# Kernel optimization log

Measured on AMD Instinct MI355X. Metric: run time of the kernel, lower is better.

## Reference

```python
import jax, jax.numpy as jnp
import numpy as np

N_NODES = 100000
N_EDGES = 1600000
F_IN = 64
C = 128          # hidden_encoding == element_embedding
STEPS = 4
NEG_SLOPE = 0.01  # torch.nn.LeakyReLU default


def setup_inputs() -> dict:
    key = jax.random.key(0)
    ks = jax.random.split(key, 8)
    s = 0.05
    return {
        "x": jax.random.normal(ks[0], (N_NODES, F_IN), dtype=jnp.float32),
        "edge_index": jax.random.randint(ks[1], (2, N_EDGES), 0, N_NODES, dtype=jnp.int64),
        "W_in": jax.random.normal(ks[2], (C, F_IN), dtype=jnp.float32) * s,
        "W_mpnn": jax.random.normal(ks[3], (STEPS, C, C), dtype=jnp.float32) * s,
        "W_ih": jax.random.normal(ks[4], (3 * C, C), dtype=jnp.float32) * s,
        "W_hh": jax.random.normal(ks[5], (3 * C, C), dtype=jnp.float32) * s,
        "b_ih": jnp.zeros((3 * C,), dtype=jnp.float32),
        "b_hh": jnp.zeros((3 * C,), dtype=jnp.float32),
        "W_pred": jax.random.normal(ks[6], (1, C), dtype=jnp.float32) * s,
        "b_pred": jnp.zeros((1,), dtype=jnp.float32),
    }


def reference(x, edge_index, W_in, W_mpnn, W_ih, W_hh, b_ih, b_hh, W_pred, b_pred):
    src, dst = edge_index[0], edge_index[1]
    n = x.shape[0]
    # input embedding (bias=False)
    h = x @ W_in.T                                  # [N, C]
    for i in range(STEPS):
        m = h @ W_mpnn[i]                           # [N, C] (PyG: matmul(x, weight[i]))
        agg = jax.ops.segment_sum(m[src], dst, num_segments=n)  # scatter-add aggr
        # torch GRUCell, gate order r, z, n
        gi = agg @ W_ih.T + b_ih                    # [N, 3C]
        gh = h @ W_hh.T + b_hh                      # [N, 3C]
        r = jax.nn.sigmoid(gi[:, :C] + gh[:, :C])
        z = jax.nn.sigmoid(gi[:, C:2 * C] + gh[:, C:2 * C])
        nn_ = jnp.tanh(gi[:, 2 * C:] + r * gh[:, 2 * C:])
        h = (1.0 - z) * nn_ + z * h
    h = jnp.where(h >= 0, h, NEG_SLOPE * h)         # LeakyReLU
    g = jnp.mean(h, axis=0)                         # graph readout [C]
    return g @ W_pred.T + b_pred                    # [1]
```

## Files before the change

### kernel.cpp

```cpp
#include <hip/hip_runtime.h>
#include <cstdint>

typedef __attribute__((ext_vector_type(8))) short bf16x8;
typedef __attribute__((ext_vector_type(4))) float f32x4;
typedef __attribute__((address_space(1))) unsigned int ga_u32;
typedef __attribute__((address_space(3))) unsigned int ls_u32;

__device__ __forceinline__ float bf2f(unsigned short u) {
    union { unsigned int i; float f; } v; v.i = ((unsigned int)u) << 16; return v.f;
}
__device__ __forceinline__ float bfhi(unsigned int w) {
    union { unsigned int i; float f; } v; v.i = w & 0xffff0000u; return v.f;
}
__device__ __forceinline__ float bflo(unsigned int w) {
    union { unsigned int i; float f; } v; v.i = w << 16; return v.f;
}
__device__ __forceinline__ unsigned short f2bf(float f) {
    union { float ff; unsigned int i; } v; v.ff = f;
    unsigned int r = (v.i + 0x7fffu + ((v.i >> 16) & 1u)) >> 16;
    return (unsigned short)r;
}
__device__ __forceinline__ int origcol(int nc) {
    int w = nc / 96, rem = nc % 96, g = rem / 32, cc = rem % 32;
    return g * 128 + w * 32 + cc;
}

__global__ void detect_kernel(const unsigned int* __restrict__ x32,
                              const int* __restrict__ ei32,
                              int* __restrict__ flags)
{
    __shared__ int insaneS;
    __shared__ int orS;
    int tid = threadIdx.x;
    if (tid == 0) { insaneS = 0; orS = 0; }
    __syncthreads();
    int insane = 0;
    for (int j = tid; j < 512; j += 256) {
        unsigned int w = x32[j];
        int e = (int)((w >> 7) & 0xFF);
        if (e > 135 || e < 100) insane++;
    }
    int ov = 0;
    for (int j = tid; j < 256; j += 256) ov |= ei32[2 * j + 1];
    atomicAdd(&insaneS, insane);
    atomicOr(&orS, ov);
    __syncthreads();
    if (tid == 0) {
        flags[0] = (insaneS < 64) ? 1 : 0;
        flags[1] = (orS == 0) ? 1 : 0;
    }
}

__global__ void convall_kernel(const void* W_in, const void* W_mpnn, const void* W_ih,
                               const void* W_hh, const void* b_ih, const void* b_hh,
                               const void* W_pred, const void* b_pred,
                               float* __restrict__ Winf, float* __restrict__ Wmf,
                               float* __restrict__ Wihf, float* __restrict__ Whhf,
                               float* __restrict__ bihf, float* __restrict__ bhhf,
                               float* __restrict__ Wpf, float* __restrict__ bpf,
                               int steps, const int* __restrict__ flags)
{
    int i = blockIdx.x * 256 + threadIdx.x;
    int bf = flags[0];
    auto get = [&](const void* p, int idx) -> float {
        return bf ? bf2f(((const unsigned short*)p)[idx]) : ((const float*)p)[idx];
    };
    int n0 = 8192, n1 = n0 + steps * 16384, n2 = n1 + 49152, n3 = n2 + 49152;
    int n4 = n3 + 384, n5 = n4 + 384, n6 = n5 + 128, n7 = n6 + 1;
    if      (i < n0) Winf[i]      = get(W_in,   i);
    else if (i < n1) Wmf[i - n0]  = get(W_mpnn, i - n0);
    else if (i < n2) Wihf[i - n1] = get(W_ih,   i - n1);
    else if (i < n3) Whhf[i - n2] = get(W_hh,   i - n2);
    else if (i < n4) bihf[i - n3] = get(b_ih,   i - n3);
    else if (i < n5) bhhf[i - n4] = get(b_hh,   i - n4);
    else if (i < n6) Wpf[i - n5]  = get(W_pred, i - n5);
    else if (i < n7) bpf[i - n6]  = get(b_pred, i - n6);
}

__global__ void wcomb_kernel(const float* __restrict__ Wm,
                             const float* __restrict__ Wih,
                             float* __restrict__ Wcomb, int steps)
{
    int i = blockIdx.x * 256 + threadIdx.x;
    int total = steps * 49152;
    if (i >= total) return;
    int step = i / 49152;
    int rem = i - step * 49152;
    int k = rem / 384;
    int j = rem - k * 384;
    const float* wm = Wm + ((long)step * 128 + k) * 128;
    const float* wi = Wih + (long)j * 128;
    float s = 0.f;
#pragma unroll 8
    for (int t = 0; t < 128; ++t) s += wm[t] * wi[t];
    Wcomb[i] = s;
}

__global__ void pack_gates(const float* __restrict__ Wcomb,
                           const float* __restrict__ Whhf,
                           const float* __restrict__ bihf, const float* __restrict__ bhhf,
                           unsigned short* __restrict__ Bci,
                           unsigned short* __restrict__ Bhh,
                           float* __restrict__ bip, float* __restrict__ bhp,
                           int steps)
{
    int i = blockIdx.x * 256 + threadIdx.x;
    int nmat = steps * 49152;
    if (i < nmat) {
        int s = i / 49152, r = i - s * 49152;
        int t = r >> 11, rem = r & 2047;
        int ks = rem >> 9, l = (rem >> 3) & 63, j = rem & 7;
        int k = ks * 32 + (l >> 4) * 8 + j;
        int oc = origcol(t * 16 + (l & 15));
        Bci[i] = f2bf(Wcomb[(long)s * 49152 + k * 384 + oc]);
    } else if (i < nmat + 49152) {
        int r = i - nmat;
        int t = r >> 11, rem = r & 2047;
        int ks = rem >> 9, l = (rem >> 3) & 63, j = rem & 7;
        int k = ks * 32 + (l >> 4) * 8 + j;
        int oc = origcol(t * 16 + (l & 15));
        Bhh[r] = f2bf(Whhf[(long)oc * 128 + k]);
    } else if (i < nmat + 49152 + 768) {
        int b = i - nmat - 49152;
        if (b < 384) bip[b] = bihf[origcol(b)];
        else         bhp[b - 384] = bhhf[origcol(b - 384)];
    }
}

__global__ void pack_in(const float* __restrict__ Winf, unsigned short* __restrict__ Bin)
{
    int r = blockIdx.x * 256 + threadIdx.x;
    if (r >= 8192) return;
    int t = r >> 10, rem = r & 1023;
    int ks = rem >> 9, l = (rem >> 3) & 63, j = rem & 7;
    int k = ks * 32 + (l >> 4) * 8 + j;
    int col = t * 16 + (l & 15);
    Bin[r] = f2bf(Winf[col * 64 + k]);
}

__global__ __launch_bounds__(256) void gemm_in(const void* __restrict__ xraw,
                        const int* __restrict__ flags,
                        const unsigned short* __restrict__ Bin,
                        unsigned short* __restrict__ hout, int N)
{
    const int w = threadIdx.x >> 6, lane = threadIdx.x & 63;
    const int m = lane & 15, quad = lane >> 4;
    const int rowBase = blockIdx.x * 32;
    const bool abf = flags[0] != 0;
    f32x4 acc[2][2];
#pragma unroll
    for (int rt = 0; rt < 2; ++rt)
#pragma unroll
        for (int ct = 0; ct < 2; ++ct) acc[rt][ct] = (f32x4){0.f, 0.f, 0.f, 0.f};

#pragma unroll
    for (int ks = 0; ks < 2; ++ks) {
        bf16x8 a[2];
#pragma unroll
        for (int rt = 0; rt < 2; ++rt) {
            long row = rowBase + rt * 16 + m;
            if (abf) {
                a[rt] = *(const bf16x8*)(const void*)((const unsigned short*)xraw + row * 64 + ks * 32 + quad * 8);
            } else {
                const float* xp = (const float*)xraw + row * 64 + ks * 32 + quad * 8;
                float4 f0 = *(const float4*)xp;
                float4 f1 = *(const float4*)(xp + 4);
                bf16x8 t;
                t[0] = (short)f2bf(f0.x); t[1] = (short)f2bf(f0.y);
                t[2] = (short)f2bf(f0.z); t[3] = (short)f2bf(f0.w);
                t[4] = (short)f2bf(f1.x); t[5] = (short)f2bf(f1.y);
                t[6] = (short)f2bf(f1.z); t[7] = (short)f2bf(f1.w);
                a[rt] = t;
            }
        }
#pragma unroll
        for (int ct = 0; ct < 2; ++ct) {
            int t = w * 2 + ct;
            bf16x8 b = *(const bf16x8*)(const void*)(Bin + ((t * 2 + ks) * 64 + lane) * 8);
#pragma unroll
            for (int rt = 0; rt < 2; ++rt)
                acc[rt][ct] = __builtin_amdgcn_mfma_f32_16x16x32_bf16(a[rt], b, acc[rt][ct], 0, 0, 0);
        }
    }
#pragma unroll
    for (int rt = 0; rt < 2; ++rt)
#pragma unroll
        for (int ct = 0; ct < 2; ++ct)
#pragma unroll
            for (int reg = 0; reg < 4; ++reg) {
                int row = rowBase + rt * 16 + quad * 4 + reg;
                int col = w * 32 + ct * 16 + m;
                if (row < N) hout[(long)row * 128 + col] = f2bf(acc[rt][ct][reg]);
            }
}

__global__ __launch_bounds__(512, 2) void step_kernel(
    const unsigned short* __restrict__ hin,
    const unsigned short* __restrict__ aggb,
    const unsigned short* __restrict__ Bci,
    const unsigned short* __restrict__ Bhh,
    const float* __restrict__ bip, const float* __restrict__ bhp,
    unsigned short* __restrict__ hout, int N, int ntiles)
{
    __shared__ unsigned short lds[16384];
    const int tid = threadIdx.x;
    const int w = tid >> 6, lane = tid & 63;
    const int m = lane & 15, quad = lane >> 4;
    const int cg = w >> 1, half = w & 1;
    const int col = cg * 32 + half * 16 + m;
    const int grid = gridDim.x;

    bf16x8 bI[4][3], bH[4][3];
#pragma unroll
    for (int ks = 0; ks < 4; ++ks)
#pragma unroll
        for (int g = 0; g < 3; ++g) {
            int t = cg * 6 + g * 2 + half;
            bI[ks][g] = *(const bf16x8*)(const void*)(Bci + (((long)t * 4 + ks) * 64 + lane) * 8);
            bH[ks][g] = *(const bf16x8*)(const void*)(Bhh + (((long)t * 4 + ks) * 64 + lane) * 8);
        }
    float bi0[3], bh0[3];
#pragma unroll
    for (int g = 0; g < 3; ++g) {
        int nc = (cg * 6 + g * 2 + half) * 16 + m;
        bi0[g] = bip[nc]; bh0[g] = bhp[nc];
    }

    const int lrow = w * 4 + (lane >> 4);
    const int schunk = (lane & 15) ^ (lrow & 7);

    long tile = blockIdx.x;
    int cur = 0;
    if (tile < ntiles) {
        const unsigned short* gap = aggb + (tile * 32 + lrow) * 128 + schunk * 8;
        const unsigned short* ghp = hin  + (tile * 32 + lrow) * 128 + schunk * 8;
        __builtin_amdgcn_global_load_lds((const ga_u32*)gap, (ls_u32*)(lds + w * 512), 16, 0, 0);
        __builtin_amdgcn_global_load_lds((const ga_u32*)ghp, (ls_u32*)(lds + 4096 + w * 512), 16, 0, 0);
    }

    for (; tile < ntiles; tile += grid) {
        long nxt = tile + grid;
        bool hasNext = nxt < ntiles;
        if (hasNext) {
            int nb = cur ^ 1;
            const unsigned short* gap = aggb + (nxt * 32 + lrow) * 128 + schunk * 8;
            const unsigned short* ghp = hin  + (nxt * 32 + lrow) * 128 + schunk * 8;
            __builtin_amdgcn_global_load_lds((const ga_u32*)gap, (ls_u32*)(lds + nb * 8192 + w * 512), 16, 0, 0);
            __builtin_amdgcn_global_load_lds((const ga_u32*)ghp, (ls_u32*)(lds + nb * 8192 + 4096 + w * 512), 16, 0, 0);
            asm volatile("s_waitcnt vmcnt(2)" ::: "memory");
        } else {
            asm volatile("s_waitcnt vmcnt(0)" ::: "memory");
        }
        __builtin_amdgcn_s_barrier();

        const unsigned short* abuf = lds + cur * 8192;
        const unsigned short* hbuf = lds + cur * 8192 + 4096;

        f32x4 gi[2][3], gh[2][3];
#pragma unroll
        for (int g = 0; g < 3; ++g)
#pragma unroll
            for (int rt = 0; rt < 2; ++rt) {
                gi[rt][g] = (f32x4){bi0[g], bi0[g], bi0[g], bi0[g]};
                gh[rt][g] = (f32x4){bh0[g], bh0[g], bh0[g], bh0[g]};
            }

#pragma unroll
        for (int ks = 0; ks < 4; ++ks) {
            bf16x8 aA[2], hA[2];
#pragma unroll
            for (int rt = 0; rt < 2; ++rt) {
                int r = rt * 16 + m;
                int ch = (ks * 4 + quad) ^ (r & 7);
                aA[rt] = *(const bf16x8*)(const void*)(abuf + r * 128 + ch * 8);
                hA[rt] = *(const bf16x8*)(const void*)(hbuf + r * 128 + ch * 8);
            }
#pragma unroll
            for (int g = 0; g < 3; ++g)
#pragma unroll
                for (int rt = 0; rt < 2; ++rt) {
                    gi[rt][g] = __builtin_amdgcn_mfma_f32_16x16x32_bf16(aA[rt], bI[ks][g], gi[rt][g], 0, 0, 0);
                    gh[rt][g] = __builtin_amdgcn_mfma_f32_16x16x32_bf16(hA[rt], bH[ks][g], gh[rt][g], 0, 0, 0);
                }
        }

        long rowBase = tile * 32;
#pragma unroll
        for (int rt = 0; rt < 2; ++rt)
#pragma unroll
            for (int reg = 0; reg < 4; ++reg) {
                long row = rowBase + rt * 16 + quad * 4 + reg;
                if (row < N) {
                    int r2 = rt * 16 + quad * 4 + reg;
                    int hidx = r2 * 128 + ((((col >> 3) ^ (r2 & 7)) << 3) + (col & 7));
                    float R  = __builtin_amdgcn_rcpf(1.f + __expf(-(gi[rt][0][reg] + gh[rt][0][reg])));
                    float Z  = __builtin_amdgcn_rcpf(1.f + __expf(-(gi[rt][1][reg] + gh[rt][1][reg])));
                    float u  = gi[rt][2][reg] + R * gh[rt][2][reg];
                    float e2 = __expf(-2.f * fabsf(u));
                    float Nn = copysignf((1.f - e2) * __builtin_amdgcn_rcpf(1.f + e2), u);
                    float hold = bf2f(hbuf[hidx]);
                    hout[row * 128 + col] = f2bf((1.f - Z) * Nn + Z * hold);
                }
            }

        __builtin_amdgcn_s_barrier();
        cur ^= 1;
    }
}

__global__ __launch_bounds__(256) void part1_kernel(
    const int* __restrict__ ei, int E, const int* __restrict__ flags,
    int* __restrict__ gcnt, uint2* __restrict__ pair2,
    int nb, int cshift, int ccap, int chunk)
{
    __shared__ int cnt[256];
    __shared__ int base_s[256];
    const int tid = threadIdx.x;
    if (tid < nb) cnt[tid] = 0;
    __syncthreads();
    const bool i64 = flags[1] != 0;
    const long long* e64 = (const long long*)ei;
    int lo = blockIdx.x * chunk;
    int hi = lo + chunk; if (hi > E) hi = E;
    for (int i = lo + tid; i < hi; i += 256) {
        int d = i64 ? (int)e64[(long)E + i] : ei[(long)E + i];
        atomicAdd(&cnt[d >> cshift], 1);
    }
    __syncthreads();
    if (tid < nb) {
        int c = cnt[tid];
        base_s[tid] = (c > 0) ? atomicAdd(&gcnt[tid], c) : 0;
        cnt[tid] = 0;
    }
    __syncthreads();
    for (int i = lo + tid; i < hi; i += 256) {
        int s, d;
        if (i64) { s = (int)e64[i]; d = (int)e64[(long)E + i]; }
        else     { s = ei[i];       d = ei[(long)E + i]; }
        int c = d >> cshift;
        int p = base_s[c] + atomicAdd(&cnt[c], 1);
        if (p < ccap) { uint2 pr; pr.x = (unsigned)s; pr.y = (unsigned)d; pair2[(long)c * ccap + p] = pr; }
    }
}

__global__ void scanco_kernel(const int* __restrict__ gcnt, int* __restrict__ cbase,
                              int nb, int ccap)
{
    __shared__ int wsum[4];
    int tid = threadIdx.x, lane = tid & 63, wv = tid >> 6;
    int x = (tid < nb) ? gcnt[tid] : 0;
    if (x > ccap) x = ccap;
    int inc = x;
#pragma unroll
    for (int d = 1; d < 64; d <<= 1) { int u = __shfl_up(inc, d); if (lane >= d) inc += u; }
    if (lane == 63) wsum[wv] = inc;
    __syncthreads();
    if (tid == 0) { int s = 0; for (int q = 0; q < 4; ++q) { int t = wsum[q]; wsum[q] = s; s += t; } }
    __syncthreads();
    int excl = wsum[wv] + inc - x;
    if (tid < nb) cbase[tid] = excl;
    if (tid == nb - 1) cbase[nb] = excl + x;
}

__global__ __launch_bounds__(256) void part2_kernel(
    const uint2* __restrict__ pair2, const int* __restrict__ gcnt,
    const int* __restrict__ cbase,
    int* __restrict__ offs, int* __restrict__ csr,
    int N, int nb, int cshift, int ccap)
{
    __shared__ int lb[2048];
    __shared__ int wsum[4];
    const int b = blockIdx.x, tid = threadIdx.x;
    const int span = 1 << cshift;
    const int n0 = b << cshift;
    int count = gcnt[b]; if (count > ccap) count = ccap;
    for (int k = tid; k < span; k += 256) lb[k] = 0;
    __syncthreads();
    const uint2* pp = pair2 + (long)b * ccap;
    for (int i = tid; i < count; i += 256)
        atomicAdd(&lb[(int)pp[i].y - n0], 1);
    __syncthreads();
    int npe = span >> 8; if (npe < 1) npe = 1;
    int myb = tid * npe;
    int vals[8];
    int sum = 0;
    for (int k = 0; k < npe; ++k) { vals[k] = lb[myb + k]; sum += vals[k]; }
    int lane = tid & 63, wv = tid >> 6;
    int inc = sum;
#pragma unroll
    for (int d = 1; d < 64; d <<= 1) { int u = __shfl_up(inc, d); if (lane >= d) inc += u; }
    if (lane == 63) wsum[wv] = inc;
    __syncthreads();
    if (tid == 0) { int s = 0; for (int q = 0; q < 4; ++q) { int t = wsum[q]; wsum[q] = s; s += t; } }
    __syncthreads();
    int run = wsum[wv] + inc - sum;
    __syncthreads();
    for (int k = 0; k < npe; ++k) { lb[myb + k] = run; run += vals[k]; }
    __syncthreads();
    int gb = cbase[b];
    int nn = N - n0; if (nn > span) nn = span;
    for (int g = tid; g < nn; g += 256) offs[n0 + g] = gb + lb[g];
    if (b == nb - 1 && tid == 0) offs[N] = cbase[nb];
    __syncthreads();
    for (int i = tid; i < count; i += 256) {
        uint2 pr = pp[i];
        int p = gb + atomicAdd(&lb[(int)pr.y - n0], 1);
        csr[p] = (int)pr.x;
    }
}

__global__ __launch_bounds__(256) void aggregate(const unsigned short* __restrict__ hb,
                          const int* __restrict__ off,
                          const int* __restrict__ csr,
                          unsigned short* __restrict__ aggb, int n)
{
    int wv = threadIdx.x >> 6, lane = threadIdx.x & 63;
    int slot = lane >> 4;
    int c16 = lane & 15;
    int nw = gridDim.x * 4;
    int wid = blockIdx.x * 4 + wv;
    int chunk = (n + nw - 1) / nw;
    int lo = wid * chunk;
    int hi = lo + chunk; if (hi > n) hi = n;

    for (int node = lo; node < hi; ++node) {
        int s0 = off[node], s1 = off[node + 1];
        float a0 = 0.f, a1 = 0.f, a2 = 0.f, a3 = 0.f, a4 = 0.f, a5 = 0.f, a6 = 0.f, a7 = 0.f;
        if (s1 > s0) {
            int last = s1 - 1;
            for (int j = s0 + slot; j < s1; j += 16) {
                uint4 vv[4];
                float wt[4];
#pragma unroll
                for (int t = 0; t < 4; ++t) {
                    int jj = j + 4 * t;
                    int idx = csr[jj <= last ? jj : last];
                    vv[t] = *(const uint4*)(const void*)(hb + (long)idx * 128 + c16 * 8);
                    wt[t] = (jj <= last) ? 1.f : 0.f;
                }
#pragma unroll
                for (int t = 0; t < 4; ++t) {
                    a0 = fmaf(bflo(vv[t].x), wt[t], a0);
                    a1 = fmaf(bfhi(vv[t].x), wt[t], a1);
                    a2 = fmaf(bflo(vv[t].y), wt[t], a2);
                    a3 = fmaf(bfhi(vv[t].y), wt[t], a3);
                    a4 = fmaf(bflo(vv[t].z), wt[t], a4);
                    a5 = fmaf(bfhi(vv[t].z), wt[t], a5);
                    a6 = fmaf(bflo(vv[t].w), wt[t], a6);
                    a7 = fmaf(bfhi(vv[t].w), wt[t], a7);
                }
            }
        }
        a0 += __shfl_xor(a0, 16); a1 += __shfl_xor(a1, 16);
        a2 += __shfl_xor(a2, 16); a3 += __shfl_xor(a3, 16);
        a4 += __shfl_xor(a4, 16); a5 += __shfl_xor(a5, 16);
        a6 += __shfl_xor(a6, 16); a7 += __shfl_xor(a7, 16);
        a0 += __shfl_xor(a0, 32); a1 += __shfl_xor(a1, 32);
        a2 += __shfl_xor(a2, 32); a3 += __shfl_xor(a3, 32);
        a4 += __shfl_xor(a4, 32); a5 += __shfl_xor(a5, 32);
        a6 += __shfl_xor(a6, 32); a7 += __shfl_xor(a7, 32);
        if (slot == 0) {
            uint4 o;
            o.x = ((unsigned int)f2bf(a1) << 16) | f2bf(a0);
            o.y = ((unsigned int)f2bf(a3) << 16) | f2bf(a2);
            o.z = ((unsigned int)f2bf(a5) << 16) | f2bf(a4);
            o.w = ((unsigned int)f2bf(a7) << 16) | f2bf(a6);
            *(uint4*)(void*)(aggb + (long)node * 128 + c16 * 8) = o;
        }
    }
}

__global__ void colsum(const unsigned short* __restrict__ hb, float* __restrict__ acc, int n) {
    int c = threadIdx.x & 127;
    int sub = threadIdx.x >> 7;
    float local = 0.f;
    for (long r = blockIdx.x * 2 + sub; r < n; r += (long)gridDim.x * 2) {
        float v = bf2f(hb[r * 128 + c]);
        local += (v >= 0.f) ? v : 0.01f * v;
    }
    atomicAdd(&acc[c], local);
}

__global__ void finalize(const float* __restrict__ acc,
                         const float* __restrict__ W_pred_f,
                         const float* __restrict__ b_pred_f,
                         unsigned int* __restrict__ out, float invN)
{
    __shared__ float ws2[2];
    int t = threadIdx.x;
    float v = acc[t] * invN * W_pred_f[t];
#pragma unroll
    for (int d = 32; d >= 1; d >>= 1) v += __shfl_down(v, d);
    if ((t & 63) == 0) ws2[t >> 6] = v;
    __syncthreads();
    if (t == 0) {
        float r = ws2[0] + ws2[1] + b_pred_f[0];
        unsigned int bf = (unsigned int)f2bf(r);
        out[0] = (bf << 16) | bf;
    }
}

extern "C" void kernel_launch(void* const* d_in, const int* in_sizes, int n_in,
                              void* d_out, int out_size, void* d_ws, size_t ws_size,
                              hipStream_t stream)
{
    const void* x      = d_in[0];
    const int*  ei     = (const int*)d_in[1];
    const void* W_in   = d_in[2];
    const void* W_mpnn = d_in[3];
    const void* W_ih   = d_in[4];
    const void* W_hh   = d_in[5];
    const void* b_ih   = d_in[6];
    const void* b_hh   = d_in[7];
    const void* W_pred = d_in[8];
    const void* b_pred = d_in[9];

    const int N = in_sizes[0] / 64;
    const int E = in_sizes[1] / 2;
    const int STEPS = in_sizes[3] / (128 * 128);

    int cshift = 9;
    while ((((N + (1 << cshift) - 1) >> cshift)) > 256 && cshift < 11) cshift++;
    const int NCO = (N + (1 << cshift) - 1) >> cshift;
    const int ccap = (((E / NCO) * 3 / 2 + 1024) + 255) & ~255;
    const int chunk = (E + 255) / 256;

    size_t woff = 0;
    auto carve = [&](size_t bytes) -> void* {
        void* p = (char*)d_ws + woff;
        woff = (woff + bytes + 255) & ~(size_t)255;
        return p;
    };
    int*   flags = (int*)carve(2 * 4);
    float* Winf  = (float*)carve(8192 * 4);
    float* Wmf   = (float*)carve((size_t)STEPS * 16384 * 4);
    float* Wihf  = (float*)carve(49152 * 4);
    float* Whhf  = (float*)carve(49152 * 4);
    float* bihf  = (float*)carve(384 * 4);
    float* bhhf  = (float*)carve(384 * 4);
    float* Wpf   = (float*)carve(128 * 4);
    float* bpf   = (float*)carve(4);
    float* Wcomb = (float*)carve((size_t)STEPS * 49152 * 4);
    unsigned short* Bci = (unsigned short*)carve((size_t)STEPS * 49152 * 2);
    unsigned short* Bhh = (unsigned short*)carve(49152 * 2);
    unsigned short* Bin = (unsigned short*)carve(8192 * 2);
    float* bip   = (float*)carve(384 * 4);
    float* bhp   = (float*)carve(384 * 4);
    unsigned short* hA   = (unsigned short*)carve(((size_t)N * 128 + 16384) * 2);
    unsigned short* hB   = (unsigned short*)carve(((size_t)N * 128 + 16384) * 2);
    unsigned short* aggb = (unsigned short*)carve(((size_t)N * 128 + 16384) * 2);
    int*   gcnt  = (int*)carve(256 * 4);
    int*   cbase = (int*)carve(257 * 4);
    int*   offs  = (int*)carve((size_t)(N + 1) * 4);
    int*   csr   = (int*)carve((size_t)E * 4 + 256);
    uint2* pair2 = (uint2*)carve((size_t)NCO * ccap * 8);
    float* accb  = (float*)carve(128 * 4);

    hipMemsetAsync(gcnt, 0, 256 * 4, stream);
    hipMemsetAsync(accb, 0, 128 * 4, stream);

    detect_kernel<<<1, 256, 0, stream>>>((const unsigned int*)x, ei, flags);

    {
        int total = 8192 + STEPS * 16384 + 2 * 49152 + 768 + 129;
        convall_kernel<<<(total + 255) / 256, 256, 0, stream>>>(
            W_in, W_mpnn, W_ih, W_hh, b_ih, b_hh, W_pred, b_pred,
            Winf, Wmf, Wihf, Whhf, bihf, bhhf, Wpf, bpf, STEPS, flags);
    }

    wcomb_kernel<<<(STEPS * 49152 + 255) / 256, 256, 0, stream>>>(Wmf, Wihf, Wcomb, STEPS);
    {
        int total = (STEPS + 1) * 49152 + 768;
        pack_gates<<<(total + 255) / 256, 256, 0, stream>>>(Wcomb, Whhf, bihf, bhhf,
                                                            Bci, Bhh, bip, bhp, STEPS);
    }
    pack_in<<<32, 256, 0, stream>>>(Winf, Bin);

    gemm_in<<<(N + 31) / 32, 256, 0, stream>>>(x, flags, Bin, hA, N);

    part1_kernel<<<256, 256, 0, stream>>>(ei, E, flags, gcnt, pair2, NCO, cshift, ccap, chunk);
    scanco_kernel<<<1, 256, 0, stream>>>(gcnt, cbase, NCO, ccap);
    part2_kernel<<<NCO, 256, 0, stream>>>(pair2, gcnt, cbase, offs, csr, N, NCO, cshift, ccap);

    int aggBlocks = (N + 3) / 4; if (aggBlocks > 2048) aggBlocks = 2048;
    const int ntiles = (N + 31) / 32;
    int stepBlocks = ntiles < 256 ? ntiles : 256;
    unsigned short* hcur = hA;
    unsigned short* hnxt = hB;
    for (int step = 0; step < STEPS; ++step) {
        aggregate<<<aggBlocks, 256, 0, stream>>>(hcur, offs, csr, aggb, N);
        step_kernel<<<stepBlocks, 512, 0, stream>>>(
            hcur, aggb, Bci + (size_t)step * 49152, Bhh, bip, bhp, hnxt, N, ntiles);
        unsigned short* t = hcur; hcur = hnxt; hnxt = t;
    }

    colsum<<<512, 256, 0, stream>>>(hcur, accb, N);
    finalize<<<1, 128, 0, stream>>>(accb, Wpf, bpf, (unsigned int*)d_out, 1.f / (float)N);
}
```

Baseline: 595.5 us.

## Fuse weight-prep, scan and finalize kernels to cut launch count

Merges detection, weight conversion, Wcomb product and packing into one prep kernel that reads raw weights directly. The block-count scan moves into part2 (each block recomputes it), and the finalize step becomes a last-block-done tail in colsum. Two memsets collapse into one. The aim is to remove about seven small kernel launches and the intermediate fp32 buffers, at the cost of redundant detection work in every prep block and redundant scans in every part2 block.

Result: no change. 602.3 us (+1.1%).

```diff
diff --git a/kernel.cpp b/kernel.cpp
--- a/kernel.cpp
+++ b/kernel.cpp
@@ -25,117 +25,104 @@
     return g * 128 + w * 32 + cc;
 }
 
-__global__ void detect_kernel(const unsigned int* __restrict__ x32,
-                              const int* __restrict__ ei32,
-                              int* __restrict__ flags)
-{
-    __shared__ int insaneS;
-    __shared__ int orS;
-    int tid = threadIdx.x;
+__global__ __launch_bounds__(256) void prep_kernel(
+    const unsigned int* __restrict__ x32, const int* __restrict__ ei32,
+    const void* W_in, const void* W_mpnn, const void* W_ih, const void* W_hh,
+    const void* b_ih, const void* b_hh, const void* W_pred, const void* b_pred,
+    unsigned short* __restrict__ Bci, unsigned short* __restrict__ Bhh,
+    float* __restrict__ bip, float* __restrict__ bhp,
+    unsigned short* __restrict__ Bin,
+    float* __restrict__ Wpf, float* __restrict__ bpf,
+    int* __restrict__ flags, int steps)
+{
+    __shared__ int insaneS, orS;
+    const int tid = threadIdx.x;
     if (tid == 0) { insaneS = 0; orS = 0; }
     __syncthreads();
-    int insane = 0;
-    for (int j = tid; j < 512; j += 256) {
-        unsigned int w = x32[j];
-        int e = (int)((w >> 7) & 0xFF);
-        if (e > 135 || e < 100) insane++;
-    }
-    int ov = 0;
-    for (int j = tid; j < 256; j += 256) ov |= ei32[2 * j + 1];
-    atomicAdd(&insaneS, insane);
-    atomicOr(&orS, ov);
-    __syncthreads();
-    if (tid == 0) {
-        flags[0] = (insaneS < 64) ? 1 : 0;
+    {
+        int insane = 0;
+        for (int j = tid; j < 512; j += 256) {
+            unsigned int w = x32[j];
+            int e = (int)((w >> 7) & 0xFF);
+            if (e > 135 || e < 100) insane++;
+        }
+        int ov = 0;
+        for (int j = tid; j < 256; j += 256) ov |= ei32[2 * j + 1];
+        atomicAdd(&insaneS, insane);
+        atomicOr(&orS, ov);
+    }
+    __syncthreads();
+    const bool bf = insaneS < 64;
+    if (blockIdx.x == 0 && tid == 0) {
+        flags[0] = bf ? 1 : 0;
         flags[1] = (orS == 0) ? 1 : 0;
     }
-}
-
-__global__ void convall_kernel(const void* W_in, const void* W_mpnn, const void* W_ih,
-                               const void* W_hh, const void* b_ih, const void* b_hh,
-                               const void* W_pred, const void* b_pred,
-                               float* __restrict__ Winf, float* __restrict__ Wmf,
-                               float* __restrict__ Wihf, float* __restrict__ Whhf,
-                               float* __restrict__ bihf, float* __restrict__ bhhf,
-                               float* __restrict__ Wpf, float* __restrict__ bpf,
-                               int steps, const int* __restrict__ flags)
-{
-    int i = blockIdx.x * 256 + threadIdx.x;
-    int bf = flags[0];
-    auto get = [&](const void* p, int idx) -> float {
+
+    auto cvt = [&](const void* p, long idx) -> float {
         return bf ? bf2f(((const unsigned short*)p)[idx]) : ((const float*)p)[idx];
     };
-    int n0 = 8192, n1 = n0 + steps * 16384, n2 = n1 + 49152, n3 = n2 + 49152;
-    int n4 = n3 + 384, n5 = n4 + 384, n6 = n5 + 128, n7 = n6 + 1;
-    if      (i < n0) Winf[i]      = get(W_in,   i);
-    else if (i < n1) Wmf[i - n0]  = get(W_mpnn, i - n0);
-    else if (i < n2) Wihf[i - n1] = get(W_ih,   i - n1);
-    else if (i < n3) Whhf[i - n2] = get(W_hh,   i - n2);
-    else if (i < n4) bihf[i - n3] = get(b_ih,   i - n3);
-    else if (i < n5) bhhf[i - n4] = get(b_hh,   i - n4);
-    else if (i < n6) Wpf[i - n5]  = get(W_pred, i - n5);
-    else if (i < n7) bpf[i - n6]  = get(b_pred, i - n6);
-}
-
-__global__ void wcomb_kernel(const float* __restrict__ Wm,
-                             const float* __restrict__ Wih,
-                             float* __restrict__ Wcomb, int steps)
-{
-    int i = blockIdx.x * 256 + threadIdx.x;
-    int total = steps * 49152;
-    if (i >= total) return;
-    int step = i / 49152;
-    int rem = i - step * 49152;
-    int k = rem / 384;
-    int j = rem - k * 384;
-    const float* wm = Wm + ((long)step * 128 + k) * 128;
-    const float* wi = Wih + (long)j * 128;
-    float s = 0.f;
-#pragma unroll 8
-    for (int t = 0; t < 128; ++t) s += wm[t] * wi[t];
-    Wcomb[i] = s;
-}
-
-__global__ void pack_gates(const float* __restrict__ Wcomb,
-                           const float* __restrict__ Whhf,
-                           const float* __restrict__ bihf, const float* __restrict__ bhhf,
-                           unsigned short* __restrict__ Bci,
-                           unsigned short* __restrict__ Bhh,
-                           float* __restrict__ bip, float* __restrict__ bhp,
-                           int steps)
-{
-    int i = blockIdx.x * 256 + threadIdx.x;
-    int nmat = steps * 49152;
-    if (i < nmat) {
-        int s = i / 49152, r = i - s * 49152;
+
+    const long n1 = (long)steps * 49152;
+    const long n2 = n1 + 49152;
+    const long n3 = n2 + 768;
+    const long n4 = n3 + 8192;
+    const long n5 = n4 + 128;
+    long i = (long)blockIdx.x * 256 + tid;
+
+    if (i < n1) {
+        int st = (int)(i / 49152), r = (int)(i - (long)st * 49152);
         int t = r >> 11, rem = r & 2047;
         int ks = rem >> 9, l = (rem >> 3) & 63, j = rem & 7;
         int k = ks * 32 + (l >> 4) * 8 + j;
         int oc = origcol(t * 16 + (l & 15));
-        Bci[i] = f2bf(Wcomb[(long)s * 49152 + k * 384 + oc]);
-    } else if (i < nmat + 49152) {
-        int r = i - nmat;
+        float s = 0.f;
+        if (bf) {
+            const unsigned short* wm = (const unsigned short*)W_mpnn + ((long)st * 128 + k) * 128;
+            const unsigned short* wi = (const unsigned short*)W_ih + (long)oc * 128;
+#pragma unroll 4
+            for (int tt = 0; tt < 128; tt += 8) {
+                uint4 a = *(const uint4*)(const void*)(wm + tt);
+                uint4 b = *(const uint4*)(const void*)(wi + tt);
+                s += bflo(a.x) * bflo(b.x) + bfhi(a.x) * bfhi(b.x);
+                s += bflo(a.y) * bflo(b.y) + bfhi(a.y) * bfhi(b.y);
+                s += bflo(a.z) * bflo(b.z) + bfhi(a.z) * bfhi(b.z);
+                s += bflo(a.w) * bflo(b.w) + bfhi(a.w) * bfhi(b.w);
+            }
+        } else {
+            const float* wm = (const float*)W_mpnn + ((long)st * 128 + k) * 128;
+            const float* wi = (const float*)W_ih + (long)oc * 128;
+#pragma unroll 4
+            for (int tt = 0; tt < 128; tt += 4) {
+                float4 a = *(const float4*)(wm + tt);
+                float4 b = *(const float4*)(wi + tt);
+                s += a.x * b.x + a.y * b.y + a.z * b.z + a.w * b.w;
+            }
+        }
+        Bci[i] = f2bf(s);
+    } else if (i < n2) {
+        int r = (int)(i - n1);
         int t = r >> 11, rem = r & 2047;
         int ks = rem >> 9, l = (rem >> 3) & 63, j = rem & 7;
         int k = ks * 32 + (l >> 4) * 8 + j;
         int oc = origcol(t * 16 + (l & 15));
-        Bhh[r] = f2bf(Whhf[(long)oc * 128 + k]);
-    } else if (i < nmat + 49152 + 768) {
-        int b = i - nmat - 49152;
-        if (b < 384) bip[b] = bihf[origcol(b)];
-        else         bhp[b - 384] = bhhf[origcol(b - 384)];
-    }
-}
-
-__global__ void pack_in(const float* __restrict__ Winf, unsigned short* __restrict__ Bin)
-{
-    int r = blockIdx.x * 256 + threadIdx.x;
-    if (r >= 8192) return;
-    int t = r >> 10, rem = r & 1023;
-    int ks = rem >> 9, l = (rem >> 3) & 63, j = rem & 7;
-    int k = ks * 32 + (l >> 4) * 8 + j;
-    int col = t * 16 + (l & 15);
-    Bin[r] = f2bf(Winf[col * 64 + k]);
+        Bhh[r] = f2bf(cvt(W_hh, (long)oc * 128 + k));
+    } else if (i < n3) {
+        int b = (int)(i - n2);
+        if (b < 384) bip[b] = cvt(b_ih, origcol(b));
+        else         bhp[b - 384] = cvt(b_hh, origcol(b - 384));
+    } else if (i < n4) {
+        int r = (int)(i - n3);
+        int t = r >> 10, rem = r & 1023;
+        int ks = rem >> 9, l = (rem >> 3) & 63, j = rem & 7;
+        int k = ks * 32 + (l >> 4) * 8 + j;
+        int col = t * 16 + (l & 15);
+        Bin[r] = f2bf(cvt(W_in, col * 64 + k));
+    } else if (i < n5) {
+        int idx = (int)(i - n4);
+        Wpf[idx] = cvt(W_pred, idx);
+    } else if (i == n5) {
+        bpf[0] = cvt(b_pred, 0);
+    }
 }
 
 __global__ __launch_bounds__(256) void gemm_in(const void* __restrict__ xraw,
@@ -343,36 +330,35 @@
     }
 }
 
-__global__ void scanco_kernel(const int* __restrict__ gcnt, int* __restrict__ cbase,
-                              int nb, int ccap)
-{
-    __shared__ int wsum[4];
-    int tid = threadIdx.x, lane = tid & 63, wv = tid >> 6;
-    int x = (tid < nb) ? gcnt[tid] : 0;
-    if (x > ccap) x = ccap;
-    int inc = x;
-#pragma unroll
-    for (int d = 1; d < 64; d <<= 1) { int u = __shfl_up(inc, d); if (lane >= d) inc += u; }
-    if (lane == 63) wsum[wv] = inc;
-    __syncthreads();
-    if (tid == 0) { int s = 0; for (int q = 0; q < 4; ++q) { int t = wsum[q]; wsum[q] = s; s += t; } }
-    __syncthreads();
-    int excl = wsum[wv] + inc - x;
-    if (tid < nb) cbase[tid] = excl;
-    if (tid == nb - 1) cbase[nb] = excl + x;
-}
-
 __global__ __launch_bounds__(256) void part2_kernel(
     const uint2* __restrict__ pair2, const int* __restrict__ gcnt,
-    const int* __restrict__ cbase,
     int* __restrict__ offs, int* __restrict__ csr,
     int N, int nb, int cshift, int ccap)
 {
     __shared__ int lb[2048];
     __shared__ int wsum[4];
+    __shared__ int cb[257];
     const int b = blockIdx.x, tid = threadIdx.x;
     const int span = 1 << cshift;
     const int n0 = b << cshift;
+    int lane = tid & 63, wv = tid >> 6;
+
+    {
+        int x = (tid < nb) ? gcnt[tid] : 0;
+        if (x > ccap) x = ccap;
+        int inc = x;
+#pragma unroll
+        for (int d = 1; d < 64; d <<= 1) { int u = __shfl_up(inc, d); if (lane >= d) inc += u; }
+        if (lane == 63) wsum[wv] = inc;
+        __syncthreads();
+        if (tid == 0) { int s = 0; for (int q = 0; q < 4; ++q) { int t = wsum[q]; wsum[q] = s; s += t; } }
+        __syncthreads();
+        int excl = wsum[wv] + inc - x;
+        if (tid < nb) cb[tid] = excl;
+        if (tid == nb - 1) cb[nb] = excl + x;
+    }
+    __syncthreads();
+
     int count = gcnt[b]; if (count > ccap) count = ccap;
     for (int k = tid; k < span; k += 256) lb[k] = 0;
     __syncthreads();
@@ -385,7 +371,6 @@
     int vals[8];
     int sum = 0;
     for (int k = 0; k < npe; ++k) { vals[k] = lb[myb + k]; sum += vals[k]; }
-    int lane = tid & 63, wv = tid >> 6;
     int inc = sum;
 #pragma unroll
     for (int d = 1; d < 64; d <<= 1) { int u = __shfl_up(inc, d); if (lane >= d) inc += u; }
@@ -397,10 +382,10 @@
     __syncthreads();
     for (int k = 0; k < npe; ++k) { lb[myb + k] = run; run += vals[k]; }
     __syncthreads();
-    int gb = cbase[b];
+    int gb = cb[b];
     int nn = N - n0; if (nn > span) nn = span;
     for (int g = tid; g < nn; g += 256) offs[n0 + g] = gb + lb[g];
-    if (b == nb - 1 && tid == 0) offs[N] = cbase[nb];
+    if (b == nb - 1 && tid == 0) offs[N] = cb[nb];
     __syncthreads();
     for (int i = tid; i < count; i += 256) {
         uint2 pr = pp[i];
@@ -470,7 +455,15 @@
     }
 }
 
-__global__ void colsum(const unsigned short* __restrict__ hb, float* __restrict__ acc, int n) {
+__global__ void colsum_fin(const unsigned short* __restrict__ hb,
+                           const float* __restrict__ Wpf,
+                           const float* __restrict__ bpf,
+                           unsigned int* __restrict__ out,
+                           float* __restrict__ acc, int* __restrict__ done,
+                           int n, float invN)
+{
+    __shared__ int isLast;
+    __shared__ float ws2[2];
     int c = threadIdx.x & 127;
     int sub = threadIdx.x >> 7;
     float local = 0.f;
@@ -479,24 +472,27 @@
         local += (v >= 0.f) ? v : 0.01f * v;
     }
     atomicAdd(&acc[c], local);
-}
-
-__global__ void finalize(const float* __restrict__ acc,
-                         const float* __restrict__ W_pred_f,
-                         const float* __restrict__ b_pred_f,
-                         unsigned int* __restrict__ out, float invN)
-{
-    __shared__ float ws2[2];
-    int t = threadIdx.x;
-    float v = acc[t] * invN * W_pred_f[t];
-#pragma unroll
-    for (int d = 32; d >= 1; d >>= 1) v += __shfl_down(v, d);
-    if ((t & 63) == 0) ws2[t >> 6] = v;
-    __syncthreads();
-    if (t == 0) {
-        float r = ws2[0] + ws2[1] + b_pred_f[0];
-        unsigned int bf = (unsigned int)f2bf(r);
-        out[0] = (bf << 16) | bf;
+    __threadfence();
+    if (threadIdx.x == 0) {
+        int d = atomicAdd(done, 1);
+        isLast = (d == (int)gridDim.x - 1) ? 1 : 0;
+    }
+    __syncthreads();
+    if (isLast) {
+        float v = 0.f;
+        if (threadIdx.x < 128) {
+            float a = atomicAdd(&acc[threadIdx.x], 0.f);
+            v = a * invN * Wpf[threadIdx.x];
+        }
+#pragma unroll
+        for (int d = 32; d >= 1; d >>= 1) v += __shfl_down(v, d);
+        if (threadIdx.x < 128 && (threadIdx.x & 63) == 0) ws2[threadIdx.x >> 6] = v;
+        __syncthreads();
+        if (threadIdx.x == 0) {
+            float r = ws2[0] + ws2[1] + bpf[0];
+            unsigned int bfv = (unsigned int)f2bf(r);
+            out[0] = (bfv << 16) | bfv;
+        }
     }
 }
 
@@ -532,15 +528,8 @@
         return p;
     };
     int*   flags = (int*)carve(2 * 4);
-    float* Winf  = (float*)carve(8192 * 4);
-    float* Wmf   = (float*)carve((size_t)STEPS * 16384 * 4);
-    float* Wihf  = (float*)carve(49152 * 4);
-    float* Whhf  = (float*)carve(49152 * 4);
-    float* bihf  = (float*)carve(384 * 4);
-    float* bhhf  = (float*)carve(384 * 4);
     float* Wpf   = (float*)carve(128 * 4);
     float* bpf   = (float*)carve(4);
-    float* Wcomb = (float*)carve((size_t)STEPS * 49152 * 4);
     unsigned short* Bci = (unsigned short*)carve((size_t)STEPS * 49152 * 2);
     unsigned short* Bhh = (unsigned short*)carve(49152 * 2);
     unsigned short* Bin = (unsigned short*)carve(8192 * 2);
@@ -549,38 +538,28 @@
     unsigned short* hA   = (unsigned short*)carve(((size_t)N * 128 + 16384) * 2);
     unsigned short* hB   = (unsigned short*)carve(((size_t)N * 128 + 16384) * 2);
     unsigned short* aggb = (unsigned short*)carve(((size_t)N * 128 + 16384) * 2);
-    int*   gcnt  = (int*)carve(256 * 4);
-    int*   cbase = (int*)carve(257 * 4);
     int*   offs  = (int*)carve((size_t)(N + 1) * 4);
     int*   csr   = (int*)carve((size_t)E * 4 + 256);
     uint2* pair2 = (uint2*)carve((size_t)NCO * ccap * 8);
+    int*   gcnt  = (int*)carve(256 * 4);
     float* accb  = (float*)carve(128 * 4);
-
-    hipMemsetAsync(gcnt, 0, 256 * 4, stream);
-    hipMemsetAsync(accb, 0, 128 * 4, stream);
-
-    detect_kernel<<<1, 256, 0, stream>>>((const unsigned int*)x, ei, flags);
+    int*   done  = (int*)carve(4);
+    size_t zbytes = (size_t)((char*)done - (char*)gcnt) + 256;
+
+    hipMemsetAsync(gcnt, 0, zbytes, stream);
 
     {
-        int total = 8192 + STEPS * 16384 + 2 * 49152 + 768 + 129;
-        convall_kernel<<<(total + 255) / 256, 256, 0, stream>>>(
-            W_in, W_mpnn, W_ih, W_hh, b_ih, b_hh, W_pred, b_pred,
-            Winf, Wmf, Wihf, Whhf, bihf, bhhf, Wpf, bpf, STEPS, flags);
-    }
-
-    wcomb_kernel<<<(STEPS * 49152 + 255) / 256, 256, 0, stream>>>(Wmf, Wihf, Wcomb, STEPS);
-    {
-        int total = (STEPS + 1) * 49152 + 768;
-        pack_gates<<<(total + 255) / 256, 256, 0, stream>>>(Wcomb, Whhf, bihf, bhhf,
-                                                            Bci, Bhh, bip, bhp, STEPS);
-    }
-    pack_in<<<32, 256, 0, stream>>>(Winf, Bin);
+        long total = (long)STEPS * 49152 + 49152 + 768 + 8192 + 128 + 1;
+        int blocks = (int)((total + 255) / 256);
+        prep_kernel<<<blocks, 256, 0, stream>>>(
+            (const unsigned int*)x, ei, W_in, W_mpnn, W_ih, W_hh, b_ih, b_hh,
+            W_pred, b_pred, Bci, Bhh, bip, bhp, Bin, Wpf, bpf, flags, STEPS);
+    }
 
     gemm_in<<<(N + 31) / 32, 256, 0, stream>>>(x, flags, Bin, hA, N);
 
     part1_kernel<<<256, 256, 0, stream>>>(ei, E, flags, gcnt, pair2, NCO, cshift, ccap, chunk);
-    scanco_kernel<<<1, 256, 0, stream>>>(gcnt, cbase, NCO, ccap);
-    part2_kernel<<<NCO, 256, 0, stream>>>(pair2, gcnt, cbase, offs, csr, N, NCO, cshift, ccap);
+    part2_kernel<<<NCO, 256, 0, stream>>>(pair2, gcnt, offs, csr, N, NCO, cshift, ccap);
 
     int aggBlocks = (N + 3) / 4; if (aggBlocks > 2048) aggBlocks = 2048;
     const int ntiles = (N + 31) / 32;
@@ -594,6 +573,6 @@
         unsigned short* t = hcur; hcur = hnxt; hnxt = t;
     }
 
-    colsum<<<512, 256, 0, stream>>>(hcur, accb, N);
-    finalize<<<1, 128, 0, stream>>>(accb, Wpf, bpf, (unsigned int*)d_out, 1.f / (float)N);
-}
+    colsum_fin<<<512, 256, 0, stream>>>(hcur, Wpf, bpf, (unsigned int*)d_out,
+                                        accb, done, N, 1.f / (float)N);
+}
```
